# Kernel tuning notes

Measured on AMD Instinct MI355X. Metric: run time of the kernel, lower is better.

The kernel has to match this reference:

```python
import jax, jax.numpy as jnp
import numpy as np

B, IN_DIM, D = 65536, 256, 32  # batch, afe.out_dim, embed_dim
LN_EPS = 1e-5


def setup_inputs() -> dict:
    key = jax.random.key(0)
    ks = jax.random.split(key, 10)
    def xavier(k, shape):
        fan_in, fan_out = shape[1], shape[0]
        lim = float(np.sqrt(6.0 / (fan_in + fan_out)))
        return jax.random.uniform(k, shape, jnp.float32, -lim, lim)
    return {
        "f1": jax.random.normal(ks[0], (B, IN_DIM), jnp.float32),
        "f4": jax.random.normal(ks[1], (B, IN_DIM), jnp.float32),
        "fD": jax.random.normal(ks[2], (B, IN_DIM), jnp.float32),
        "Wp": xavier(ks[3], (D, IN_DIM)), "bp": jnp.zeros((D,), jnp.float32),
        "ln_g": jnp.ones((D,), jnp.float32), "ln_b": jnp.zeros((D,), jnp.float32),
        "Wq": xavier(ks[4], (D, D)), "bq": jnp.zeros((D,), jnp.float32),
        "Wk": xavier(ks[5], (D, D)), "bk": jnp.zeros((D,), jnp.float32),
        "Wv": xavier(ks[6], (D, D)), "bv": jnp.zeros((D,), jnp.float32),
        "Wo1": xavier(ks[7], (D, D)), "bo1": jnp.zeros((D,), jnp.float32),
        "Wo2": xavier(ks[8], (D, D)), "bo2": jnp.zeros((D,), jnp.float32),
    }


def reference(f1, f4, fD, Wp, bp, ln_g, ln_b, Wq, bq, Wk, bk, Wv, bv, Wo1, bo1, Wo2, bo2):
    def proj(f):  # Linear -> ReLU -> LayerNorm (Dropout is identity in inference)
        h = jax.nn.relu(f @ Wp.T + bp)                      # [B, D]
        mu = jnp.mean(h, axis=-1, keepdims=True)
        var = jnp.mean((h - mu) ** 2, axis=-1, keepdims=True)
        return ln_g * (h - mu) * jax.lax.rsqrt(var + LN_EPS) + ln_b

    X = jnp.stack([proj(f1), proj(f4), proj(fD)], axis=1)   # [B, 3, D]
    Q = X @ Wq.T + bq
    K = X @ Wk.T + bk
    V = X @ Wv.T + bv
    scores = jnp.einsum("bsd,btd->bst", Q, K) / jnp.sqrt(jnp.float32(D))
    w = jax.nn.softmax(scores, axis=-1)                     # [B, 3, 3]
    attended = jnp.einsum("bst,btd->bsd", w, V)             # [B, 3, D]
    pooled = jnp.mean(attended, axis=1)                     # [B, D]
    out = jax.nn.relu(pooled @ Wo1.T + bo1) @ Wo2.T + bo2 + pooled
    return out
```

## Files before the change

### kernel.cpp

```cpp
#include <hip/hip_runtime.h>

#define BLOCK 512
#define RPB   64
#define WPH   132
#define WS    36

#define FMA4(ACC_, X_, W_) \
    ACC_ = fmaf((X_).x, (W_).x, ACC_); ACC_ = fmaf((X_).y, (W_).y, ACC_); \
    ACC_ = fmaf((X_).z, (W_).z, ACC_); ACC_ = fmaf((X_).w, (W_).w, ACC_);

__device__ __forceinline__ void matvec32(const float* __restrict__ WL, const int o,
                                         const float* __restrict__ in, float* __restrict__ outv)
{
    #pragma unroll
    for (int e = 0; e < 4; ++e) outv[e] = 0.f;
    #pragma unroll
    for (int p = 0; p < 8; ++p) {
        float xs[4];
        #pragma unroll
        for (int jj = 0; jj < 4; ++jj)
            xs[jj] = (p == 0) ? in[jj] : __shfl_xor(in[jj], p);
        const float* wb = WL + o * WS + (o ^ p) * 4;
        #pragma unroll
        for (int e = 0; e < 4; ++e) {
            float4 w = *(const float4*)(wb + e * (8 * WS));
            float t = outv[e];
            t = fmaf(w.x, xs[0], t); t = fmaf(w.y, xs[1], t);
            t = fmaf(w.z, xs[2], t); t = fmaf(w.w, xs[3], t);
            outv[e] = t;
        }
    }
}

__global__ void __launch_bounds__(BLOCK)
msfe_kernel(
    const float* __restrict__ f1, const float* __restrict__ f4, const float* __restrict__ fD,
    const float* __restrict__ Wp, const float* __restrict__ bp,
    const float* __restrict__ ln_g, const float* __restrict__ ln_b,
    const float* __restrict__ Wq, const float* __restrict__ bq,
    const float* __restrict__ Wk, const float* __restrict__ bk,
    const float* __restrict__ Wv, const float* __restrict__ bv,
    const float* __restrict__ Wo1, const float* __restrict__ bo1,
    const float* __restrict__ Wo2, const float* __restrict__ bo2,
    float* __restrict__ out, int nRows)
{
    __shared__ float Wp_l[32 * WPH];
    __shared__ float A_l[32 * WS];
    __shared__ float Wv_l[32 * WS], Wo1_l[32 * WS], Wo2_l[32 * WS];
    __shared__ float bp_l[32], g_l[32], b_l[32], u_l[32], v_l[32];
    __shared__ float bv_l[32], bo1_l[32], bo2_l[32];
    __shared__ float c_l;

    const int tid = threadIdx.x;
    const float isq = 0.17677669529663688f;

    if (tid < 256) {
        int d = tid >> 3, j4 = tid & 7;
        int base = d * WS + 16 * (j4 & 1) + (j4 >> 1);
        float4 wv = ((const float4*)Wv )[tid];
        float4 w1 = ((const float4*)Wo1)[tid];
        float4 w2 = ((const float4*)Wo2)[tid];
        Wv_l [base] = wv.x; Wv_l [base+4] = wv.y; Wv_l [base+8] = wv.z; Wv_l [base+12] = wv.w;
        Wo1_l[base] = w1.x; Wo1_l[base+4] = w1.y; Wo1_l[base+8] = w1.z; Wo1_l[base+12] = w1.w;
        Wo2_l[base] = w2.x; Wo2_l[base+4] = w2.y; Wo2_l[base+8] = w2.z; Wo2_l[base+12] = w2.w;
        float s0 = 0.f, s1 = 0.f, s2 = 0.f, s3 = 0.f;
        #pragma unroll 8
        for (int dd = 0; dd < 32; ++dd) {
            float  wq = Wq[dd * 32 + d];
            float4 wk = *(const float4*)&Wk[dd * 32 + 4 * j4];
            s0 = fmaf(wq, wk.x, s0); s1 = fmaf(wq, wk.y, s1);
            s2 = fmaf(wq, wk.z, s2); s3 = fmaf(wq, wk.w, s3);
        }
        A_l[base] = s0 * isq; A_l[base+4] = s1 * isq; A_l[base+8] = s2 * isq; A_l[base+12] = s3 * isq;
    } else if (tid < 288) {
        int a = tid - 256; float s = 0.f;
        #pragma unroll 8
        for (int d = 0; d < 32; ++d) s = fmaf(bq[d], Wk[d * 32 + a], s);
        u_l[a] = s * isq;
    } else if (tid < 320) {
        int a = tid - 288; float s = 0.f;
        #pragma unroll 8
        for (int d = 0; d < 32; ++d) s = fmaf(Wq[d * 32 + a], bk[d], s);
        v_l[a] = s * isq;
    } else if (tid == 320) {
        float s = 0.f;
        #pragma unroll 8
        for (int d = 0; d < 32; ++d) s = fmaf(bq[d], bk[d], s);
        c_l = s * isq;
    } else if (tid >= 480) {
        int a = tid - 480;
        bp_l[a] = bp[a]; g_l[a] = ln_g[a]; b_l[a] = ln_b[a];
    } else if (tid >= 448) {
        int a = tid - 448;
        bv_l[a] = bv[a]; bo1_l[a] = bo1[a]; bo2_l[a] = bo2[a];
    }

    const int o = tid & 7;
    int row = blockIdx.x * RPB + (tid >> 3);
    const bool active = (row < nRows);
    if (!active) row = nRows - 1;

    const size_t rowoff = (size_t)row * 256;
    const float* wbase = &Wp_l[o * WPH];

    float acc0[4], acc1[4], acc2[4];
    #pragma unroll
    for (int e = 0; e < 4; ++e) { acc0[e] = 0.f; acc1[e] = 0.f; acc2[e] = 0.f; }

    #pragma unroll
    for (int h = 0; h < 2; ++h) {
        if (h) __syncthreads();
        #pragma unroll
        for (int i = 0; i < 2; ++i) {
            int idx = tid + i * BLOCK;
            int d = idx >> 5, k4 = idx & 31;
            *(float4*)&Wp_l[d * WPH + 4 * k4] = ((const float4*)Wp)[d * 64 + 32 * h + k4];
        }
        __syncthreads();

        const float* __restrict__ b0 = f1 + rowoff + 128 * h;
        const float* __restrict__ b1 = f4 + rowoff + 128 * h;
        const float* __restrict__ b2 = fD + rowoff + 128 * h;

        float4 X0 = *(const float4*)(b0),     X1 = *(const float4*)(b1),     X2 = *(const float4*)(b2);
        float4 Y0 = *(const float4*)(b0 + 4), Y1 = *(const float4*)(b1 + 4), Y2 = *(const float4*)(b2 + 4);

        #pragma unroll 1
        for (int kc = 0; kc < 128; kc += 8) {
            {
                const float* wr = wbase + kc;
                #pragma unroll
                for (int e = 0; e < 4; ++e) {
                    float4 w = *(const float4*)(wr + e * (8 * WPH));
                    FMA4(acc0[e], X0, w) FMA4(acc1[e], X1, w) FMA4(acc2[e], X2, w)
                }
            }
            if (kc + 8 < 128) {
                X0 = *(const float4*)(b0 + kc + 8);
                X1 = *(const float4*)(b1 + kc + 8);
                X2 = *(const float4*)(b2 + kc + 8);
            }
            {
                const float* wr = wbase + kc + 4;
                #pragma unroll
                for (int e = 0; e < 4; ++e) {
                    float4 w = *(const float4*)(wr + e * (8 * WPH));
                    FMA4(acc0[e], Y0, w) FMA4(acc1[e], Y1, w) FMA4(acc2[e], Y2, w)
                }
            }
            if (kc + 12 < 128) {
                Y0 = *(const float4*)(b0 + kc + 12);
                Y1 = *(const float4*)(b1 + kc + 12);
                Y2 = *(const float4*)(b2 + kc + 12);
            }
        }
    }

    float Xh[3][4];
    float bpe[4], ge[4], be[4];
    #pragma unroll
    for (int e = 0; e < 4; ++e) { bpe[e] = bp_l[o + 8*e]; ge[e] = g_l[o + 8*e]; be[e] = b_l[o + 8*e]; }
    #pragma unroll
    for (int s = 0; s < 3; ++s) {
        float* accp = (s == 0) ? acc0 : (s == 1) ? acc1 : acc2;
        float sm = 0.f, sq = 0.f;
        #pragma unroll
        for (int e = 0; e < 4; ++e) {
            float t = fmaxf(accp[e] + bpe[e], 0.f);
            accp[e] = t; sm += t; sq = fmaf(t, t, sq);
        }
        sm += __shfl_xor(sm, 1); sm += __shfl_xor(sm, 2); sm += __shfl_xor(sm, 4);
        sq += __shfl_xor(sq, 1); sq += __shfl_xor(sq, 2); sq += __shfl_xor(sq, 4);
        float mu  = sm * 0.03125f;
        float var = fmaf(-mu, mu, sq * 0.03125f);
        float inv = rsqrtf(var + 1e-5f);
        #pragma unroll
        for (int e = 0; e < 4; ++e)
            Xh[s][e] = fmaf(ge[e] * (accp[e] - mu), inv, be[e]);
    }

    float uX[3], vX[3];
    {
        float uq[4], vq[4];
        #pragma unroll
        for (int e = 0; e < 4; ++e) { uq[e] = u_l[o + 8*e]; vq[e] = v_l[o + 8*e]; }
        #pragma unroll
        for (int t = 0; t < 3; ++t) {
            float us = 0.f, vs = 0.f;
            #pragma unroll
            for (int e = 0; e < 4; ++e) {
                us = fmaf(uq[e], Xh[t][e], us);
                vs = fmaf(vq[e], Xh[t][e], vs);
            }
            us += __shfl_xor(us, 1); us += __shfl_xor(us, 2); us += __shfl_xor(us, 4);
            vs += __shfl_xor(vs, 1); vs += __shfl_xor(vs, 2); vs += __shfl_xor(vs, 4);
            uX[t] = us; vX[t] = vs;
        }
    }

    float sc[9];
    #pragma unroll
    for (int t = 0; t < 3; ++t) {
        float y[4];
        matvec32(A_l, o, Xh[t], y);
        #pragma unroll
        for (int s = 0; s < 3; ++s) {
            float p = 0.f;
            #pragma unroll
            for (int e = 0; e < 4; ++e) p = fmaf(Xh[s][e], y[e], p);
            sc[s * 3 + t] = p;
        }
    }
    #pragma unroll
    for (int s = 0; s < 3; ++s)
        #pragma unroll
        for (int t = 0; t < 3; ++t) {
            float p = sc[s * 3 + t];
            p += __shfl_xor(p, 1); p += __shfl_xor(p, 2); p += __shfl_xor(p, 4);
            sc[s * 3 + t] = p + uX[t] + vX[s] + c_l;
        }

    float g0 = 0.f, g1 = 0.f, g2 = 0.f;
    #pragma unroll
    for (int s = 0; s < 3; ++s) {
        float a0 = sc[s*3+0], a1 = sc[s*3+1], a2 = sc[s*3+2];
        float m  = fmaxf(a0, fmaxf(a1, a2));
        float e0 = __expf(a0 - m), e1 = __expf(a1 - m), e2 = __expf(a2 - m);
        float r  = 1.f / (e0 + e1 + e2);
        g0 = fmaf(e0, r, g0); g1 = fmaf(e1, r, g1); g2 = fmaf(e2, r, g2);
    }
    g0 *= (1.f/3.f); g1 *= (1.f/3.f); g2 *= (1.f/3.f);

    float xb[4];
    #pragma unroll
    for (int e = 0; e < 4; ++e)
        xb[e] = fmaf(g0, Xh[0][e], fmaf(g1, Xh[1][e], g2 * Xh[2][e]));

    float t8[4], ph[4], hh[4];
    matvec32(Wv_l, o, xb, t8);
    #pragma unroll
    for (int e = 0; e < 4; ++e) ph[e] = t8[e] + bv_l[o + 8 * e];
    matvec32(Wo1_l, o, ph, t8);
    #pragma unroll
    for (int e = 0; e < 4; ++e) hh[e] = fmaxf(t8[e] + bo1_l[o + 8 * e], 0.f);
    matvec32(Wo2_l, o, hh, t8);

    float fin[4];
    #pragma unroll
    for (int e = 0; e < 4; ++e) fin[e] = t8[e] + bo2_l[o + 8 * e] + ph[e];

    const int sb = 4 * (o & 1);
    float ov[4];
    #pragma unroll
    for (int i = 0; i < 4; ++i) {
        float c0 = __shfl(fin[0], sb + i, 8);
        float c1 = __shfl(fin[1], sb + i, 8);
        float c2 = __shfl(fin[2], sb + i, 8);
        float c3 = __shfl(fin[3], sb + i, 8);
        float lo = (o & 2) ? c1 : c0;
        float hi = (o & 2) ? c3 : c2;
        ov[i] = (o & 4) ? hi : lo;
    }
    if (active)
        *(float4*)(out + (size_t)row * 32 + 4 * o) = make_float4(ov[0], ov[1], ov[2], ov[3]);
}

extern "C" void kernel_launch(void* const* d_in, const int* in_sizes, int n_in,
                              void* d_out, int out_size, void* d_ws, size_t ws_size,
                              hipStream_t stream) {
    const float* f1   = (const float*)d_in[0];
    const float* f4   = (const float*)d_in[1];
    const float* fD   = (const float*)d_in[2];
    const float* Wp   = (const float*)d_in[3];
    const float* bp   = (const float*)d_in[4];
    const float* ln_g = (const float*)d_in[5];
    const float* ln_b = (const float*)d_in[6];
    const float* Wq   = (const float*)d_in[7];
    const float* bq   = (const float*)d_in[8];
    const float* Wk   = (const float*)d_in[9];
    const float* bk   = (const float*)d_in[10];
    const float* Wv   = (const float*)d_in[11];
    const float* bv   = (const float*)d_in[12];
    const float* Wo1  = (const float*)d_in[13];
    const float* bo1  = (const float*)d_in[14];
    const float* Wo2  = (const float*)d_in[15];
    const float* bo2  = (const float*)d_in[16];

    const int nRows  = in_sizes[0] / 256;
    const int blocks = (nRows + RPB - 1) / RPB;

    msfe_kernel<<<blocks, BLOCK, 0, stream>>>(
        f1, f4, fD, Wp, bp, ln_g, ln_b, Wq, bq, Wk, bk, Wv, bv,
        Wo1, bo1, Wo2, bo2, (float*)d_out, nRows);
}
```

Baseline: 276.3 us.

## Use packed FP32 FMA for projection and matvecs, prefetch across halves

Replaces scalar fmaf accumulation with two-wide packed vector FMAs (v_pk_fma_f32) in both the 256-wide projection and the 32x32 matvecs, halving the FMA instruction count. The matvec gathers change from xor shuffles to rotated indexed shuffles, which also spreads LDS weight reads across banks. The two-half loop is unrolled by hand so the second half's first input loads are issued before the barrier and weight reload. The cost is extra accumulator registers and a final horizontal add, plus a different summation order.

```diff
diff --git a/kernel.cpp b/kernel.cpp
--- a/kernel.cpp
+++ b/kernel.cpp
@@ -5,31 +5,49 @@
 #define WPH   132
 #define WS    36
 
-#define FMA4(ACC_, X_, W_) \
-    ACC_ = fmaf((X_).x, (W_).x, ACC_); ACC_ = fmaf((X_).y, (W_).y, ACC_); \
-    ACC_ = fmaf((X_).z, (W_).z, ACC_); ACC_ = fmaf((X_).w, (W_).w, ACC_);
+typedef float v2f __attribute__((ext_vector_type(2)));
+
+#define PK(ACC_, A_, B_) ACC_ = __builtin_elementwise_fma(A_, B_, ACC_)
+
+#define CHUNK4(WR_, X0_, X1_, X2_) do {                                         \
+    _Pragma("unroll")                                                           \
+    for (int e = 0; e < 4; ++e) {                                               \
+        const float4 w = *(const float4*)((WR_) + e * (8 * WPH));               \
+        const v2f wlo = {w.x, w.y}, whi = {w.z, w.w};                           \
+        { const v2f xl = {(X0_).x, (X0_).y}, xh = {(X0_).z, (X0_).w};           \
+          PK(pa0[e], xl, wlo); PK(pa0[e], xh, whi); }                           \
+        { const v2f xl = {(X1_).x, (X1_).y}, xh = {(X1_).z, (X1_).w};           \
+          PK(pa1[e], xl, wlo); PK(pa1[e], xh, whi); }                           \
+        { const v2f xl = {(X2_).x, (X2_).y}, xh = {(X2_).z, (X2_).w};           \
+          PK(pa2[e], xl, wlo); PK(pa2[e], xh, whi); }                           \
+    }                                                                           \
+} while (0)
 
 __device__ __forceinline__ void matvec32(const float* __restrict__ WL, const int o,
+                                         const int lbase,
                                          const float* __restrict__ in, float* __restrict__ outv)
 {
-    #pragma unroll
-    for (int e = 0; e < 4; ++e) outv[e] = 0.f;
+    v2f o2[4];
+    #pragma unroll
+    for (int e = 0; e < 4; ++e) o2[e] = (v2f){0.f, 0.f};
     #pragma unroll
     for (int p = 0; p < 8; ++p) {
+        const int g = (o + p) & 7;
         float xs[4];
         #pragma unroll
         for (int jj = 0; jj < 4; ++jj)
-            xs[jj] = (p == 0) ? in[jj] : __shfl_xor(in[jj], p);
-        const float* wb = WL + o * WS + (o ^ p) * 4;
+            xs[jj] = (p == 0) ? in[jj] : __shfl(in[jj], lbase + g);
+        const v2f xlo = {xs[0], xs[1]}, xhi = {xs[2], xs[3]};
+        const float* wb = WL + o * WS + g * 4;
         #pragma unroll
         for (int e = 0; e < 4; ++e) {
-            float4 w = *(const float4*)(wb + e * (8 * WS));
-            float t = outv[e];
-            t = fmaf(w.x, xs[0], t); t = fmaf(w.y, xs[1], t);
-            t = fmaf(w.z, xs[2], t); t = fmaf(w.w, xs[3], t);
-            outv[e] = t;
-        }
-    }
+            const float4 w = *(const float4*)(wb + e * (8 * WS));
+            const v2f wlo = {w.x, w.y}, whi = {w.z, w.w};
+            PK(o2[e], wlo, xlo); PK(o2[e], whi, xhi);
+        }
+    }
+    #pragma unroll
+    for (int e = 0; e < 4; ++e) outv[e] = o2[e][0] + o2[e][1];
 }
 
 __global__ void __launch_bounds__(BLOCK)
@@ -95,65 +113,83 @@
         bv_l[a] = bv[a]; bo1_l[a] = bo1[a]; bo2_l[a] = bo2[a];
     }
 
-    const int o = tid & 7;
+    const int o     = tid & 7;
+    const int lbase = (tid & 63) & ~7;
     int row = blockIdx.x * RPB + (tid >> 3);
     const bool active = (row < nRows);
     if (!active) row = nRows - 1;
 
     const size_t rowoff = (size_t)row * 256;
+    const float* __restrict__ b0 = f1 + rowoff;
+    const float* __restrict__ b1 = f4 + rowoff;
+    const float* __restrict__ b2 = fD + rowoff;
     const float* wbase = &Wp_l[o * WPH];
 
+    v2f pa0[4], pa1[4], pa2[4];
+    #pragma unroll
+    for (int e = 0; e < 4; ++e) { pa0[e] = (v2f){0.f,0.f}; pa1[e] = (v2f){0.f,0.f}; pa2[e] = (v2f){0.f,0.f}; }
+
+    #pragma unroll
+    for (int i = 0; i < 2; ++i) {
+        int idx = tid + i * BLOCK;
+        int d = idx >> 5, k4 = idx & 31;
+        *(float4*)&Wp_l[d * WPH + 4 * k4] = ((const float4*)Wp)[d * 64 + k4];
+    }
+    __syncthreads();
+
+    float4 X0 = *(const float4*)(b0),     X1 = *(const float4*)(b1),     X2 = *(const float4*)(b2);
+    float4 Y0 = *(const float4*)(b0 + 4), Y1 = *(const float4*)(b1 + 4), Y2 = *(const float4*)(b2 + 4);
+
+    #pragma unroll 1
+    for (int kc = 0; kc < 128; kc += 8) {
+        CHUNK4(wbase + kc, X0, X1, X2);
+        if (kc + 8 < 128) {
+            X0 = *(const float4*)(b0 + kc + 8);
+            X1 = *(const float4*)(b1 + kc + 8);
+            X2 = *(const float4*)(b2 + kc + 8);
+        }
+        CHUNK4(wbase + kc + 4, Y0, Y1, Y2);
+        if (kc + 12 < 128) {
+            Y0 = *(const float4*)(b0 + kc + 12);
+            Y1 = *(const float4*)(b1 + kc + 12);
+            Y2 = *(const float4*)(b2 + kc + 12);
+        }
+    }
+
+    X0 = *(const float4*)(b0 + 128); X1 = *(const float4*)(b1 + 128); X2 = *(const float4*)(b2 + 128);
+    Y0 = *(const float4*)(b0 + 132); Y1 = *(const float4*)(b1 + 132); Y2 = *(const float4*)(b2 + 132);
+
+    __syncthreads();
+    #pragma unroll
+    for (int i = 0; i < 2; ++i) {
+        int idx = tid + i * BLOCK;
+        int d = idx >> 5, k4 = idx & 31;
+        *(float4*)&Wp_l[d * WPH + 4 * k4] = ((const float4*)Wp)[d * 64 + 32 + k4];
+    }
+    __syncthreads();
+
+    #pragma unroll 1
+    for (int kc = 0; kc < 128; kc += 8) {
+        CHUNK4(wbase + kc, X0, X1, X2);
+        if (kc + 8 < 128) {
+            X0 = *(const float4*)(b0 + 136 + kc);
+            X1 = *(const float4*)(b1 + 136 + kc);
+            X2 = *(const float4*)(b2 + 136 + kc);
+        }
+        CHUNK4(wbase + kc + 4, Y0, Y1, Y2);
+        if (kc + 12 < 128) {
+            Y0 = *(const float4*)(b0 + 140 + kc);
+            Y1 = *(const float4*)(b1 + 140 + kc);
+            Y2 = *(const float4*)(b2 + 140 + kc);
+        }
+    }
+
     float acc0[4], acc1[4], acc2[4];
     #pragma unroll
-    for (int e = 0; e < 4; ++e) { acc0[e] = 0.f; acc1[e] = 0.f; acc2[e] = 0.f; }
-
-    #pragma unroll
-    for (int h = 0; h < 2; ++h) {
-        if (h) __syncthreads();
-        #pragma unroll
-        for (int i = 0; i < 2; ++i) {
-            int idx = tid + i * BLOCK;
-            int d = idx >> 5, k4 = idx & 31;
-            *(float4*)&Wp_l[d * WPH + 4 * k4] = ((const float4*)Wp)[d * 64 + 32 * h + k4];
-        }
-        __syncthreads();
-
-        const float* __restrict__ b0 = f1 + rowoff + 128 * h;
-        const float* __restrict__ b1 = f4 + rowoff + 128 * h;
-        const float* __restrict__ b2 = fD + rowoff + 128 * h;
-
-        float4 X0 = *(const float4*)(b0),     X1 = *(const float4*)(b1),     X2 = *(const float4*)(b2);
-        float4 Y0 = *(const float4*)(b0 + 4), Y1 = *(const float4*)(b1 + 4), Y2 = *(const float4*)(b2 + 4);
-
-        #pragma unroll 1
-        for (int kc = 0; kc < 128; kc += 8) {
-            {
-                const float* wr = wbase + kc;
-                #pragma unroll
-                for (int e = 0; e < 4; ++e) {
-                    float4 w = *(const float4*)(wr + e * (8 * WPH));
-                    FMA4(acc0[e], X0, w) FMA4(acc1[e], X1, w) FMA4(acc2[e], X2, w)
-                }
-            }
-            if (kc + 8 < 128) {
-                X0 = *(const float4*)(b0 + kc + 8);
-                X1 = *(const float4*)(b1 + kc + 8);
-                X2 = *(const float4*)(b2 + kc + 8);
-            }
-            {
-                const float* wr = wbase + kc + 4;
-                #pragma unroll
-                for (int e = 0; e < 4; ++e) {
-                    float4 w = *(const float4*)(wr + e * (8 * WPH));
-                    FMA4(acc0[e], Y0, w) FMA4(acc1[e], Y1, w) FMA4(acc2[e], Y2, w)
-                }
-            }
-            if (kc + 12 < 128) {
-                Y0 = *(const float4*)(b0 + kc + 12);
-                Y1 = *(const float4*)(b1 + kc + 12);
-                Y2 = *(const float4*)(b2 + kc + 12);
-            }
-        }
+    for (int e = 0; e < 4; ++e) {
+        acc0[e] = pa0[e][0] + pa0[e][1];
+        acc1[e] = pa1[e][0] + pa1[e][1];
+        acc2[e] = pa2[e][0] + pa2[e][1];
     }
 
     float Xh[3][4];
@@ -202,7 +238,7 @@
     #pragma unroll
     for (int t = 0; t < 3; ++t) {
         float y[4];
-        matvec32(A_l, o, Xh[t], y);
+        matvec32(A_l, o, lbase, Xh[t], y);
         #pragma unroll
         for (int s = 0; s < 3; ++s) {
             float p = 0.f;
@@ -237,13 +273,13 @@
         xb[e] = fmaf(g0, Xh[0][e], fmaf(g1, Xh[1][e], g2 * Xh[2][e]));
 
     float t8[4], ph[4], hh[4];
-    matvec32(Wv_l, o, xb, t8);
+    matvec32(Wv_l, o, lbase, xb, t8);
     #pragma unroll
     for (int e = 0; e < 4; ++e) ph[e] = t8[e] + bv_l[o + 8 * e];
-    matvec32(Wo1_l, o, ph, t8);
+    matvec32(Wo1_l, o, lbase, ph, t8);
     #pragma unroll
     for (int e = 0; e < 4; ++e) hh[e] = fmaxf(t8[e] + bo1_l[o + 8 * e], 0.f);
-    matvec32(Wo2_l, o, hh, t8);
+    matvec32(Wo2_l, o, lbase, hh, t8);
 
     float fin[4];
     #pragma unroll
```

After: 290.3 us. 5.1% more time.
